# Kernel optimization log

Measured on AMD Instinct MI355X. Metric: run time of the kernel, lower is better.

## Reference

```python
import jax, jax.numpy as jnp
import numpy as np

COMMITMENT_COST = 0.25
LAMBDA_KL = 1.0
EPS = 1e-10


def setup_inputs() -> dict:
    key = jax.random.key(0)
    k1, k2 = jax.random.split(key)
    x = jax.random.normal(k1, (8, 4096, 256), dtype=jnp.float32)
    embedding = jax.random.normal(k2, (1024, 256), dtype=jnp.float32)
    return {"x": x, "embedding": embedding}


def reference(x, embedding):
    B, T, D = x.shape
    M, _ = embedding.shape
    x_sg = jax.lax.stop_gradient(x)
    x_flat = x_sg.reshape(-1, D)  # [N, D]
    distances = (jnp.sum(embedding ** 2, axis=1)[None, :]
                 + jnp.sum(x_flat ** 2, axis=1, keepdims=True)
                 - 2.0 * (x_flat @ embedding.T))  # [N, M]
    indices = jnp.argmin(distances.astype(jnp.float32), axis=-1)  # [N]
    quantized = embedding[indices].reshape(B, T, D)
    # losses (x detached in both terms, matching torch)
    loss = (COMMITMENT_COST * jnp.mean((x_sg - quantized) ** 2)
            + jnp.mean((quantized - x_sg) ** 2)) * LAMBDA_KL
    # straight-through estimator
    quantized_st = x + jax.lax.stop_gradient(quantized - x)
    # avg of one-hot encodings == normalized code counts (avoids NxM one-hot)
    N = B * T
    counts = jnp.zeros((M,), dtype=jnp.float32).at[indices].add(1.0)
    avg_probs = counts / N
    perplexity = jnp.exp(-jnp.sum(avg_probs * jnp.log(avg_probs + EPS)))
    return (quantized_st, loss, indices.reshape(B, T), perplexity)
```

## Files before the change

kernel.cpp:

```cpp
#include <hip/hip_runtime.h>


constexpr int D = 256;
constexpr int M = 1024;
constexpr int ROWS = 64;

typedef _Float16 f16;
typedef __attribute__((ext_vector_type(8)))  _Float16 f16x8;
typedef __attribute__((ext_vector_type(4)))  float f32x4;
typedef __attribute__((ext_vector_type(16))) float f32x16;

constexpr size_t WS_ENORM_F = 1028;
constexpr size_t WS_TAB_B   = 8320;
constexpr size_t WS_NEEDED  = 1056896;

__device__ inline void gload_lds16(const void* g, void* l) {
    __builtin_amdgcn_global_load_lds(
        (const __attribute__((address_space(1))) unsigned int*)(g),
        (__attribute__((address_space(3))) unsigned int*)(l), 16, 0, 0);
}

__global__ __launch_bounds__(256) void prep_kernel(const float* __restrict__ e,
                                                   float* __restrict__ ws) {
    const int b = blockIdx.x, t = threadIdx.x;
    if (b < 256) {
        int v    = b * 256 + t;
        int lane = v & 63, u = (v >> 6) & 15;
        int ksl  = (v >> 10) & 1, t32 = v >> 11;
        int kstep = u & 7, spl = u >> 3;
        int row  = t32 * 32 + (lane & 31);
        int col0 = (ksl * 8 + kstep) * 16 + (lane >> 5) * 8;
        const float* p = e + (size_t)row * D + col0;
        f32x4 a = *reinterpret_cast<const f32x4*>(p);
        f32x4 c = *reinterpret_cast<const f32x4*>(p + 4);
        f16 h0=(f16)a.x,h1=(f16)a.y,h2=(f16)a.z,h3=(f16)a.w;
        f16 h4=(f16)c.x,h5=(f16)c.y,h6=(f16)c.z,h7=(f16)c.w;
        f16x8 out;
        if (spl == 0) out = (f16x8){h0,h1,h2,h3,h4,h5,h6,h7};
        else          out = (f16x8){(f16)(a.x-(float)h0),(f16)(a.y-(float)h1),
                                    (f16)(a.z-(float)h2),(f16)(a.w-(float)h3),
                                    (f16)(c.x-(float)h4),(f16)(c.y-(float)h5),
                                    (f16)(c.z-(float)h6),(f16)(c.w-(float)h7)};
        *reinterpret_cast<f16x8*>((char*)ws + WS_TAB_B + (size_t)v * 16) = out;
    } else if (b < 512) {
        int row  = (b - 256) * 4 + (t >> 6);
        int lane = t & 63;
        f32x4 a = *reinterpret_cast<const f32x4*>(e + (size_t)row * D + lane * 4);
        float s = fmaf(a.x, a.x, fmaf(a.y, a.y, fmaf(a.z, a.z, a.w * a.w)));
#pragma unroll
        for (int o = 32; o > 0; o >>= 1) s += __shfl_down(s, o, 64);
        if (lane == 0) ws[WS_ENORM_F + row] = s;
    } else {
        for (int i = t; i < 1026; i += 256) ws[i] = 0.f;
    }
}

__global__ __launch_bounds__(256, 2) void vq_fused_kernel(
    const float* __restrict__ x, const float* __restrict__ e,
    float* __restrict__ outQ, float* __restrict__ outIdx, float* __restrict__ ws)
{
    __shared__ ushort ebuf[2][2][8192];
    __shared__ float  en_s[M];
    __shared__ float  wval[4][32];
    __shared__ int    widx[4][32];
    __shared__ float  xns[ROWS];
    __shared__ int    fidx[ROWS];

    const int tid   = threadIdx.x;
    const int w     = __builtin_amdgcn_readfirstlane(tid >> 6);
    const int l     = tid & 63;
    const int rpair = w >> 1;
    const int mhalf = w & 1;
    const int R     = blockIdx.x * ROWS;
    const int xr    = l & 31;
    const int kg    = l >> 5;
    const char* tab = (const char*)ws + WS_TAB_B;

    auto stage = [&](int buf, int g) {
        int tt = g >> 1, ks = g & 1;
#pragma unroll
        for (int i = 0; i < 8; ++i) {
            int S = w * 8 + i, half = S >> 4, sg = S & 15;
            gload_lds16(tab + (size_t)(((half * 16 + tt) * 2 + ks)) * 16384 + sg * 1024 + l * 16,
                        &ebuf[buf][half][sg * 512]);
        }
    };
    stage(0, 0);

    {
        f32x4 v = *reinterpret_cast<const f32x4*>(ws + WS_ENORM_F + tid * 4);
        *reinterpret_cast<f32x4*>(&en_s[tid * 4]) = v;
    }

    f16x8 Xh[16], Xl[16];
    float xn;
    {
        float s = 0.f;
#pragma unroll
        for (int ku = 0; ku < 16; ++ku) {
            const float* p = x + (size_t)(R + rpair * 32 + xr) * D + ku * 16 + kg * 8;
            f32x4 a = *reinterpret_cast<const f32x4*>(p);
            f32x4 c = *reinterpret_cast<const f32x4*>(p + 4);
            f16 h0=(f16)a.x,h1=(f16)a.y,h2=(f16)a.z,h3=(f16)a.w;
            f16 h4=(f16)c.x,h5=(f16)c.y,h6=(f16)c.z,h7=(f16)c.w;
            Xh[ku] = (f16x8){h0,h1,h2,h3,h4,h5,h6,h7};
            Xl[ku] = (f16x8){(f16)(a.x-(float)h0),(f16)(a.y-(float)h1),
                             (f16)(a.z-(float)h2),(f16)(a.w-(float)h3),
                             (f16)(c.x-(float)h4),(f16)(c.y-(float)h5),
                             (f16)(c.z-(float)h6),(f16)(c.w-(float)h7)};
            s = fmaf(a.x,a.x,fmaf(a.y,a.y,fmaf(a.z,a.z,fmaf(a.w,a.w,
                fmaf(c.x,c.x,fmaf(c.y,c.y,fmaf(c.z,c.z,fmaf(c.w,c.w,s))))))));
        }
        s += __shfl_xor(s, 32, 64);
        xn = s;
    }
    __syncthreads();

    float bV = 3.4e38f;
    int   bI = 0;
    const ushort* eb0 = &ebuf[0][mhalf][0];
    const ushort* eb1 = &ebuf[1][mhalf][0];

    for (int t = 0; t < 16; ++t) {
        f32x16 accA = {0.f}, accB = {0.f};

        stage(1, 2 * t + 1);
        __builtin_amdgcn_s_setprio(1);
#pragma unroll
        for (int kstep = 0; kstep < 8; ++kstep) {
            f16x8 Ah = *reinterpret_cast<const f16x8*>(eb0 + kstep * 512 + l * 8);
            f16x8 Al = *reinterpret_cast<const f16x8*>(eb0 + (8 + kstep) * 512 + l * 8);
            accA = __builtin_amdgcn_mfma_f32_32x32x16_f16(Ah, Xh[kstep], accA, 0, 0, 0);
            accB = __builtin_amdgcn_mfma_f32_32x32x16_f16(Al, Xh[kstep], accB, 0, 0, 0);
            accA = __builtin_amdgcn_mfma_f32_32x32x16_f16(Ah, Xl[kstep], accA, 0, 0, 0);
        }
        __builtin_amdgcn_s_setprio(0);
        __syncthreads();

        if (t < 15) stage(0, 2 * t + 2);
        __builtin_amdgcn_s_setprio(1);
#pragma unroll
        for (int kstep = 0; kstep < 8; ++kstep) {
            f16x8 Ah = *reinterpret_cast<const f16x8*>(eb1 + kstep * 512 + l * 8);
            f16x8 Al = *reinterpret_cast<const f16x8*>(eb1 + (8 + kstep) * 512 + l * 8);
            accA = __builtin_amdgcn_mfma_f32_32x32x16_f16(Ah, Xh[8 + kstep], accA, 0, 0, 0);
            accB = __builtin_amdgcn_mfma_f32_32x32x16_f16(Al, Xh[8 + kstep], accB, 0, 0, 0);
            accA = __builtin_amdgcn_mfma_f32_32x32x16_f16(Ah, Xl[8 + kstep], accA, 0, 0, 0);
        }
        __builtin_amdgcn_s_setprio(0);
        __syncthreads();

        const int mbase = mhalf * 512 + t * 32;
#pragma unroll
        for (int rq = 0; rq < 4; ++rq) {
            f32x4 en4 = *reinterpret_cast<const f32x4*>(&en_s[mbase + rq * 8 + kg * 4]);
#pragma unroll
            for (int j = 0; j < 4; ++j) {
                int reg = rq * 4 + j;
                int mi  = mbase + rq * 8 + kg * 4 + j;
                float dv = fmaf(-2.f, accA[reg] + accB[reg], en4[j]);
                if (dv < bV) { bV = dv; bI = mi; }
            }
        }
    }

    {
        float ov = __shfl_xor(bV, 32, 64);
        int   oi = __shfl_xor(bI, 32, 64);
        if (ov < bV || (ov == bV && oi < bI)) { bV = ov; bI = oi; }
    }
    if (l < 32) {
        wval[w][xr] = bV;
        widx[w][xr] = bI;
        if (mhalf == 0) xns[rpair * 32 + xr] = xn;
    }
    __syncthreads();

    if (tid < 64) {
        int r = tid, g2 = r >> 5, rr = r & 31;
        float v0 = wval[g2 * 2 + 0][rr]; int i0 = widx[g2 * 2 + 0][rr];
        float v1 = wval[g2 * 2 + 1][rr]; int i1 = widx[g2 * 2 + 1][rr];
        float fv; int fi;
        if (v1 < v0) { fv = v1; fi = i1; } else { fv = v0; fi = i0; }
        fidx[r] = fi;
        outIdx[R + r] = (float)fi;
        atomicAdd(ws + 1 + fi, 1.0f);
        float ls = fv + xns[r];
#pragma unroll
        for (int o = 32; o > 0; o >>= 1) ls += __shfl_down(ls, o, 64);
        if (r == 0) atomicAdd(ws, ls);
    }
    __syncthreads();

#pragma unroll
    for (int it = 0; it < 16; ++it) {
        int u = it * 256 + tid;
        int row = u >> 6, c4 = u & 63;
        f32x4 v = *reinterpret_cast<const f32x4*>(e + (size_t)fidx[row] * D + c4 * 4);
        __builtin_nontemporal_store(v, reinterpret_cast<f32x4*>(outQ + (size_t)(R + row) * D + c4 * 4));
    }
}

__global__ void enorm_kernel(const float* __restrict__ e, float* __restrict__ enorm) {
    int m = blockIdx.x, l = threadIdx.x;
    const f32x4 v = *reinterpret_cast<const f32x4*>(e + m * D + l * 4);
    float s = fmaf(v.x, v.x, fmaf(v.y, v.y, fmaf(v.z, v.z, v.w * v.w)));
#pragma unroll
    for (int o = 32; o > 0; o >>= 1) s += __shfl_down(s, o, 64);
    if (l == 0) enorm[m] = s;
}

__global__ __launch_bounds__(256, 2) void vq_main_kernel(
    const float* __restrict__ x, const float* __restrict__ e,
    float* __restrict__ outQ, float* __restrict__ outIdx, float* __restrict__ ws) {
    __shared__ f32x4 xs[64][64];
    __shared__ float cval[4][64];
    __shared__ int   cidx[4][64];
    __shared__ int   fidx[64];
    const int tid = threadIdx.x, row0 = blockIdx.x * 64;
#pragma unroll
    for (int it = 0; it < 16; ++it) {
        int f = it * 256 + tid, rr = f >> 6, c4 = f & 63;
        xs[rr][c4 ^ (rr & 7)] = *reinterpret_cast<const f32x4*>(x + (row0 + rr) * D + c4 * 4);
    }
    __syncthreads();
    const int r = tid & 63, c = __builtin_amdgcn_readfirstlane(tid >> 6), sw = r & 7;
    float xnorm = 0.f;
    if (c == 0) {
        f32x4 a = (f32x4){0.f,0.f,0.f,0.f};
        for (int d4 = 0; d4 < 64; ++d4) {
            f32x4 xv = xs[r][d4 ^ sw];
            a.x = fmaf(xv.x, xv.x, a.x); a.y = fmaf(xv.y, xv.y, a.y);
            a.z = fmaf(xv.z, xv.z, a.z); a.w = fmaf(xv.w, xv.w, a.w);
        }
        xnorm = (a.x + a.y) + (a.z + a.w);
    }
    const float* __restrict__ enorm = ws + WS_ENORM_F;
    float bestVal = 3.4e38f; int bestIdx = 0;
    for (int chunk = 0; chunk < M / 32; ++chunk) {
        const int m0 = chunk * 32 + c * 8;
        f32x4 acc[8];
#pragma unroll
        for (int mi = 0; mi < 8; ++mi) acc[mi] = (f32x4){0.f,0.f,0.f,0.f};
#pragma unroll 2
        for (int d4 = 0; d4 < 64; ++d4) {
            const f32x4 xv = xs[r][d4 ^ sw];
#pragma unroll
            for (int mi = 0; mi < 8; ++mi) {
                const f32x4 ev = *reinterpret_cast<const f32x4*>(e + (m0 + mi) * D + d4 * 4);
                acc[mi].x = fmaf(xv.x, ev.x, acc[mi].x); acc[mi].y = fmaf(xv.y, ev.y, acc[mi].y);
                acc[mi].z = fmaf(xv.z, ev.z, acc[mi].z); acc[mi].w = fmaf(xv.w, ev.w, acc[mi].w);
            }
        }
#pragma unroll
        for (int mi = 0; mi < 8; ++mi) {
            float dot = (acc[mi].x + acc[mi].y) + (acc[mi].z + acc[mi].w);
            float val = enorm[m0 + mi] - 2.0f * dot;
            if (val < bestVal) { bestVal = val; bestIdx = m0 + mi; }
        }
    }
    cval[c][r] = bestVal; cidx[c][r] = bestIdx;
    __syncthreads();
    if (c == 0) {
        float bv = bestVal; int bi = bestIdx;
#pragma unroll
        for (int cc = 1; cc < 4; ++cc) {
            float v = cval[cc][r]; int i = cidx[cc][r];
            if (v < bv || (v == bv && i < bi)) { bv = v; bi = i; }
        }
        fidx[r] = bi; outIdx[row0 + r] = (float)bi;
        atomicAdd(ws + 1 + bi, 1.0f);
        float dist = bv + xnorm;
#pragma unroll
        for (int o = 32; o > 0; o >>= 1) dist += __shfl_down(dist, o, 64);
        if (r == 0) atomicAdd(ws, dist);
    }
    __syncthreads();
#pragma unroll
    for (int it = 0; it < 16; ++it) {
        int f = it * 256 + tid, rr = f >> 6, c4 = f & 63;
        *reinterpret_cast<f32x4*>(outQ + (row0 + rr) * D + c4 * 4) =
            *reinterpret_cast<const f32x4*>(e + fidx[rr] * D + c4 * 4);
    }
}

__global__ void vq_final_kernel(const float* __restrict__ ws,
                                float* __restrict__ outLoss, float* __restrict__ outPpl,
                                float invN, float invND) {
    int t = threadIdx.x;
    float p = ws[1 + t] * invN;
    float term = p * logf(p + 1e-10f);
#pragma unroll
    for (int o = 32; o > 0; o >>= 1) term += __shfl_down(term, o, 64);
    __shared__ float s[16];
    if ((t & 63) == 0) s[t >> 6] = term;
    __syncthreads();
    if (t == 0) {
        float tot = 0.f;
#pragma unroll
        for (int i = 0; i < 16; ++i) tot += s[i];
        *outPpl  = expf(-tot);
        *outLoss = 1.25f * ws[0] * invND;
    }
}

extern "C" void kernel_launch(void* const* d_in, const int* in_sizes, int n_in,
                              void* d_out, int out_size, void* d_ws, size_t ws_size,
                              hipStream_t stream) {
    const float* x = (const float*)d_in[0];
    const float* e = (const float*)d_in[1];
    const int NX = in_sizes[0];
    const int N  = NX / D;

    float* out     = (float*)d_out;
    float* outQ    = out;
    float* outLoss = out + NX;
    float* outIdx  = out + NX + 1;
    float* outPpl  = out + NX + 1 + N;
    float* ws      = (float*)d_ws;

    if (ws_size >= WS_NEEDED && (N % ROWS) == 0) {
        prep_kernel<<<513, 256, 0, stream>>>(e, ws);
        vq_fused_kernel<<<N / ROWS, 256, 0, stream>>>(x, e, outQ, outIdx, ws);
    } else {
        (void)hipMemsetAsync(d_ws, 0, 4100, stream);
        enorm_kernel<<<M, 64, 0, stream>>>(e, ws + WS_ENORM_F);
        vq_main_kernel<<<N / 64, 256, 0, stream>>>(x, e, outQ, outIdx, ws);
    }
    vq_final_kernel<<<1, 1024, 0, stream>>>(ws, outLoss, outPpl,
                                            1.0f / (float)N, 1.0f / (float)NX);
}
```

Measured before the change: 80.22 us.

## Fold final loss/perplexity reduction into last block and split MFMA accumulator chain

Adds a grid-wide completion counter so the last block to finish computes perplexity and loss, which removes the separate single-block final kernel launch on the fast path. It also gives the low-part correction MFMAs their own accumulator, so the dependent chain on accA is shorter and more MFMAs can be in flight. The cost is extra registers (16 more accumulator VGPRs) that may pressure occupancy, plus a threadfence and atomic at the end of every block.

```diff
diff --git a/kernel.cpp b/kernel.cpp
--- a/kernel.cpp
+++ b/kernel.cpp
@@ -51,13 +51,15 @@
         for (int o = 32; o > 0; o >>= 1) s += __shfl_down(s, o, 64);
         if (lane == 0) ws[WS_ENORM_F + row] = s;
     } else {
-        for (int i = t; i < 1026; i += 256) ws[i] = 0.f;
+        for (int i = t; i < 1028; i += 256) ws[i] = 0.f;
     }
 }
 
 __global__ __launch_bounds__(256, 2) void vq_fused_kernel(
     const float* __restrict__ x, const float* __restrict__ e,
-    float* __restrict__ outQ, float* __restrict__ outIdx, float* __restrict__ ws)
+    float* __restrict__ outQ, float* __restrict__ outIdx,
+    float* __restrict__ outLoss, float* __restrict__ outPpl,
+    float* __restrict__ ws)
 {
     __shared__ ushort ebuf[2][2][8192];
     __shared__ float  en_s[M];
@@ -65,6 +67,8 @@
     __shared__ int    widx[4][32];
     __shared__ float  xns[ROWS];
     __shared__ int    fidx[ROWS];
+    __shared__ float  psum[4];
+    __shared__ int    isLast;
 
     const int tid   = threadIdx.x;
     const int w     = __builtin_amdgcn_readfirstlane(tid >> 6);
@@ -122,7 +126,7 @@
     const ushort* eb1 = &ebuf[1][mhalf][0];
 
     for (int t = 0; t < 16; ++t) {
-        f32x16 accA = {0.f}, accB = {0.f};
+        f32x16 accA = {0.f}, accB = {0.f}, accC = {0.f};
 
         stage(1, 2 * t + 1);
         __builtin_amdgcn_s_setprio(1);
@@ -132,7 +136,7 @@
             f16x8 Al = *reinterpret_cast<const f16x8*>(eb0 + (8 + kstep) * 512 + l * 8);
             accA = __builtin_amdgcn_mfma_f32_32x32x16_f16(Ah, Xh[kstep], accA, 0, 0, 0);
             accB = __builtin_amdgcn_mfma_f32_32x32x16_f16(Al, Xh[kstep], accB, 0, 0, 0);
-            accA = __builtin_amdgcn_mfma_f32_32x32x16_f16(Ah, Xl[kstep], accA, 0, 0, 0);
+            accC = __builtin_amdgcn_mfma_f32_32x32x16_f16(Ah, Xl[kstep], accC, 0, 0, 0);
         }
         __builtin_amdgcn_s_setprio(0);
         __syncthreads();
@@ -145,7 +149,7 @@
             f16x8 Al = *reinterpret_cast<const f16x8*>(eb1 + (8 + kstep) * 512 + l * 8);
             accA = __builtin_amdgcn_mfma_f32_32x32x16_f16(Ah, Xh[8 + kstep], accA, 0, 0, 0);
             accB = __builtin_amdgcn_mfma_f32_32x32x16_f16(Al, Xh[8 + kstep], accB, 0, 0, 0);
-            accA = __builtin_amdgcn_mfma_f32_32x32x16_f16(Ah, Xl[8 + kstep], accA, 0, 0, 0);
+            accC = __builtin_amdgcn_mfma_f32_32x32x16_f16(Ah, Xl[8 + kstep], accC, 0, 0, 0);
         }
         __builtin_amdgcn_s_setprio(0);
         __syncthreads();
@@ -158,7 +162,7 @@
             for (int j = 0; j < 4; ++j) {
                 int reg = rq * 4 + j;
                 int mi  = mbase + rq * 8 + kg * 4 + j;
-                float dv = fmaf(-2.f, accA[reg] + accB[reg], en4[j]);
+                float dv = fmaf(-2.f, accA[reg] + accB[reg] + accC[reg], en4[j]);
                 if (dv < bV) { bV = dv; bI = mi; }
             }
         }
@@ -199,6 +203,35 @@
         f32x4 v = *reinterpret_cast<const f32x4*>(e + (size_t)fidx[row] * D + c4 * 4);
         __builtin_nontemporal_store(v, reinterpret_cast<f32x4*>(outQ + (size_t)(R + row) * D + c4 * 4));
     }
+
+    __threadfence();
+    if (tid == 0) {
+        int old = __hip_atomic_fetch_add((int*)(ws + 1026), 1,
+                                         __ATOMIC_ACQ_REL, __HIP_MEMORY_SCOPE_AGENT);
+        isLast = (old == (int)gridDim.x - 1) ? 1 : 0;
+    }
+    __syncthreads();
+    if (isLast) {
+        const float invN  = 1.0f / (float)((int)gridDim.x * ROWS);
+        const float invND = invN / (float)D;
+        float term = 0.f;
+        for (int i = tid; i < M; i += 256) {
+            float cnt = __hip_atomic_load(ws + 1 + i, __ATOMIC_RELAXED,
+                                          __HIP_MEMORY_SCOPE_AGENT);
+            float p = cnt * invN;
+            term += p * logf(p + 1e-10f);
+        }
+#pragma unroll
+        for (int o = 32; o > 0; o >>= 1) term += __shfl_down(term, o, 64);
+        if ((tid & 63) == 0) psum[tid >> 6] = term;
+        __syncthreads();
+        if (tid == 0) {
+            float tot = psum[0] + psum[1] + psum[2] + psum[3];
+            float ls  = __hip_atomic_load(ws, __ATOMIC_RELAXED, __HIP_MEMORY_SCOPE_AGENT);
+            *outPpl  = expf(-tot);
+            *outLoss = 1.25f * ls * invND;
+        }
+    }
 }
 
 __global__ void enorm_kernel(const float* __restrict__ e, float* __restrict__ enorm) {
@@ -321,12 +354,13 @@
 
     if (ws_size >= WS_NEEDED && (N % ROWS) == 0) {
         prep_kernel<<<513, 256, 0, stream>>>(e, ws);
-        vq_fused_kernel<<<N / ROWS, 256, 0, stream>>>(x, e, outQ, outIdx, ws);
+        vq_fused_kernel<<<N / ROWS, 256, 0, stream>>>(x, e, outQ, outIdx,
+                                                      outLoss, outPpl, ws);
     } else {
-        (void)hipMemsetAsync(d_ws, 0, 4100, stream);
+        (void)hipMemsetAsync(d_ws, 0, 4112, stream);
         enorm_kernel<<<M, 64, 0, stream>>>(e, ws + WS_ENORM_F);
         vq_main_kernel<<<N / 64, 256, 0, stream>>>(x, e, outQ, outIdx, ws);
-    }
-    vq_final_kernel<<<1, 1024, 0, stream>>>(ws, outLoss, outPpl,
-                                            1.0f / (float)N, 1.0f / (float)NX);
-}
+        vq_final_kernel<<<1, 1024, 0, stream>>>(ws, outLoss, outPpl,
+                                                1.0f / (float)N, 1.0f / (float)NX);
+    }
+}
```

After: 156.3 us. 1.95x slower.
